# Optimization experiments

Measured on AMD Instinct MI355X. Metric: run time of the kernel, lower is better.

The kernel has to match this reference:

```python
import jax, jax.numpy as jnp
import numpy as np

N_NODES = 20000
L_MAX = 6
R_IN = 256
R_HID = 512
R_OUT = 256
LEAKY_SLOPE = 0.01  # torch.nn.functional.leaky_relu default


def setup_inputs() -> dict:
    key = jax.random.key(0)
    k1, k2, k3, k4 = jax.random.split(key, 4)
    x = jax.random.normal(k1, (N_NODES, R_IN, L_MAX * 2), dtype=jnp.float32)
    # per-node rotation angles -> per-degree 2x2 rotation matrices (k*theta for degree k)
    theta = jax.random.uniform(k2, (N_NODES,), dtype=jnp.float32, minval=0.0, maxval=2.0 * np.pi)
    ang = theta[:, None] * jnp.arange(1, L_MAX + 1, dtype=jnp.float32)[None, :]  # (n, L)
    c, s = jnp.cos(ang), jnp.sin(ang)
    rot_theta = jnp.stack([jnp.stack([c, -s], axis=-1),
                           jnp.stack([s, c], axis=-1)], axis=-2)  # (n, L, 2, 2)
    # xavier_normal: std = sqrt(2 / (fan_in + fan_out))
    W1 = jax.random.normal(k3, (L_MAX, R_HID, R_IN), dtype=jnp.float32) * np.sqrt(2.0 / (R_IN + R_HID))
    W2 = jax.random.normal(k4, (L_MAX, R_OUT, R_HID), dtype=jnp.float32) * np.sqrt(2.0 / (R_HID + R_OUT))
    return {"x": x, "rot_theta": rot_theta, "W1": W1, "W2": W2}


def so2_linear(x, W, r_out):
    # x: (n, r_in, L_max*2); W: (L_max, r_out, r_in)
    n = x.shape[0]
    x4 = x.reshape(n, -1, L_MAX, 2)              # (n, r_in, L, 2)
    out = jnp.einsum('nilc,loi->nolc', x4, W)    # fused block-diagonal GEMM over degrees
    return out.reshape(n, r_out, L_MAX * 2)


def rot_activation(x, rot):
    # rotate each degree-l 2-vector into local frame, apply leaky_relu, rotate back
    n = x.shape[0]
    x4 = x.reshape(n, -1, L_MAX, 2)                      # (n, r, L, 2)
    a = jnp.einsum('njlm,nlmc->njlc', x4, rot)           # x @ R per (node, degree)
    a = jnp.where(a >= 0, a, LEAKY_SLOPE * a)            # pointwise leaky_relu
    out = jnp.einsum('njlc,nlmc->njlm', a, rot)          # (act) @ R^T  (inverse rotation)
    return out.reshape(x.shape)


def reference(x, rot_theta, W1, W2):
    h = so2_linear(x, W1, R_HID)
    h = rot_activation(h, rot_theta)
    return so2_linear(h, W2, R_OUT)
```

## Files before the change

### kernel.cpp

```cpp
#include <hip/hip_runtime.h>
#include <stdint.h>


#define LMAX 6
#define NN 20000
#define RIN 256
#define RHID 512
#define ROUT 256
#define MTILE 64
#define NMT 626
#define MPAD (NMT*MTILE)

typedef __attribute__((ext_vector_type(8))) short short8;
typedef __attribute__((ext_vector_type(16))) float f32x16;

__device__ __forceinline__ uint16_t f2bf(float f) {
  uint32_t x = __builtin_bit_cast(uint32_t, f);
  x += 0x7fffu + ((x >> 16) & 1u);
  return (uint16_t)(x >> 16);
}
__device__ __forceinline__ float bf2f(uint16_t u) {
  return __builtin_bit_cast(float, ((uint32_t)u) << 16);
}

__device__ __forceinline__ f32x16 mfma32(short8 a, short8 b, f32x16 c) {
  return __builtin_amdgcn_mfma_f32_32x32x16_bf16(a, b, c, 0, 0, 0);
}

__device__ __forceinline__ int swz512(int row, int colb) {
  return row * 512 + ((((colb >> 4) ^ row) & 31) << 4) + (colb & 15);
}

__global__ void prep_weights(const float* __restrict__ W1, const float* __restrict__ W2,
                             uint16_t* __restrict__ w1f, uint16_t* __restrict__ w2f) {
  int idx = blockIdx.x * 256 + threadIdx.x;
  if (idx >= LMAX * RHID * RIN) return;
  {
    int l = idx / (RHID * RIN);
    int rem = idx - l * (RHID * RIN);
    int o = rem >> 8;
    int i = rem & 255;
    int lane = ((i >> 3) & 1) * 32 + (o & 31);
    size_t dst = (size_t)l * (RHID * RIN) +
                 ((((size_t)(o >> 5) * 16 + (i >> 4)) * 64 + lane) * 8 + (i & 7));
    w1f[dst] = f2bf(W1[idx]);
  }
  {
    int l = idx / (ROUT * RHID);
    int rem = idx - l * (ROUT * RHID);
    int o = rem >> 9;
    int j = rem & 511;
    int lane = ((j >> 3) & 1) * 32 + (o & 31);
    size_t dst = (size_t)l * (ROUT * RHID) +
                 ((((size_t)(o >> 5) * 32 + (j >> 4)) * 64 + lane) * 8 + (j & 7));
    w2f[dst] = f2bf(W2[idx]);
  }
}

__global__ void prep_x(const float* __restrict__ x, const float* __restrict__ rot,
                       uint16_t* __restrict__ xr) {
  int t = blockIdx.x * 256 + threadIdx.x;
  if (t >= NN * RIN) return;
  int n = t >> 8, i = t & 255;
  const float4* xp = (const float4*)(x + (size_t)t * 12);
  float4 v0 = xp[0], v1 = xp[1], v2 = xp[2];
  float xv[12] = {v0.x, v0.y, v0.z, v0.w, v1.x, v1.y, v1.z, v1.w, v2.x, v2.y, v2.z, v2.w};
  const float* rp = rot + (size_t)n * 24;
#pragma unroll
  for (int l = 0; l < LMAX; ++l) {
    float c0 = xv[2 * l], c1 = xv[2 * l + 1];
    float r00 = rp[4 * l + 0], r01 = rp[4 * l + 1];
    float r10 = rp[4 * l + 2], r11 = rp[4 * l + 3];
    float a0 = c0 * r00 + c1 * r10;
    float a1 = c0 * r01 + c1 * r11;
    size_t base = (size_t)l * MPAD * RIN + (size_t)(2 * n) * RIN + i;
    xr[base] = f2bf(a0);
    xr[base + RIN] = f2bf(a1);
  }
}

__global__ __launch_bounds__(512, 4) void so2_gemm(
    const uint16_t* __restrict__ xr,
    const uint16_t* __restrict__ w1f,
    const uint16_t* __restrict__ w2f,
    uint16_t* __restrict__ g) {
  __shared__ alignas(16) uint8_t Xs[MTILE * 512];
  __shared__ alignas(16) uint8_t A2[MTILE * 512];

  const int l = blockIdx.y;
  const int m0 = blockIdx.x * MTILE;
  const int tid = threadIdx.x;
  const int lane = tid & 63;
  const int wid = tid >> 6;
  const int l31 = lane & 31;
  const int lh = lane >> 5;
  const int wm = wid & 1;
  const int wn4 = wid >> 1;

  const uint16_t* w1p = w1f + (size_t)l * (RHID * RIN);
  const uint16_t* w2p = w2f + (size_t)l * (ROUT * RHID);

  const char* xsrc = (const char*)(xr + (size_t)l * MPAD * RIN + (size_t)m0 * RIN);
#pragma unroll
  for (int it = 0; it < 4; ++it) {
    int off = it * 8192 + tid * 16;
    int row = off >> 9;
    int colb = off & 511;
    short8 v = __builtin_nontemporal_load((const short8*)(xsrc + off));
    *(short8*)(Xs + swz512(row, colb)) = v;
  }
  __syncthreads();

  f32x16 acc1[2];
  f32x16 acc2[2];
#pragma unroll
  for (int a = 0; a < 2; ++a) acc2[a] = (f32x16)(0.f);

  auto G1 = [&](int oc) {
#pragma unroll
    for (int a = 0; a < 2; ++a) acc1[a] = (f32x16)(0.f);
    const uint16_t* wc = w1p + (size_t)(oc * 8 + wid) * (16 * 64 * 8);
#pragma unroll 4
    for (int ks = 0; ks < 16; ++ks) {
      short8 b = *(const short8*)(wc + ((size_t)ks * 64 + lane) * 8);
#pragma unroll
      for (int mf = 0; mf < 2; ++mf) {
        int row = mf * 32 + l31;
        short8 a = *(const short8*)(Xs + swz512(row, ks * 32 + lh * 16));
        acc1[mf] = mfma32(a, b, acc1[mf]);
      }
    }
  };

  auto WA2 = [&]() {
#pragma unroll
    for (int mf = 0; mf < 2; ++mf)
#pragma unroll
      for (int r = 0; r < 16; ++r) {
        int row = mf * 32 + (r & 3) + 8 * (r >> 2) + 4 * lh;
        int colb = (wid * 32 + l31) * 2;
        float v = acc1[mf][r];
        v = v >= 0.f ? v : 0.01f * v;
        *(uint16_t*)(A2 + swz512(row, colb)) = f2bf(v);
      }
  };

  auto G2 = [&](int oc) {
#pragma unroll 4
    for (int ks = 0; ks < 16; ++ks) {
      int row = wm * 32 + l31;
      short8 a = *(const short8*)(A2 + swz512(row, ks * 32 + lh * 16));
#pragma unroll
      for (int nf = 0; nf < 2; ++nf) {
        short8 b = *(const short8*)(w2p +
            ((size_t)((wn4 * 2 + nf) * 32 + oc * 16 + ks) * 64 + lane) * 8);
        acc2[nf] = mfma32(a, b, acc2[nf]);
      }
    }
  };

  G1(0);
  WA2();
  __syncthreads();
  G2(0);
  G1(1);
  __syncthreads();
  WA2();
  __syncthreads();
  G2(1);

#pragma unroll
  for (int nf = 0; nf < 2; ++nf)
#pragma unroll
    for (int r = 0; r < 16; ++r) {
      int row = wm * 32 + (r & 3) + 8 * (r >> 2) + 4 * lh;
      int colb = ((wn4 * 2 + nf) * 32 + l31) * 2;
      *(uint16_t*)(Xs + swz512(row, colb)) = f2bf(acc2[nf][r]);
    }
  __syncthreads();

  char* gdst = (char*)(g + (size_t)l * MPAD * ROUT + (size_t)m0 * ROUT);
#pragma unroll
  for (int it = 0; it < 4; ++it) {
    int off = it * 8192 + tid * 16;
    int row = off >> 9;
    int colb = off & 511;
    short8 v = *(const short8*)(Xs + swz512(row, colb));
    __builtin_nontemporal_store(v, (short8*)(gdst + off));
  }
}

__global__ void post_out(const uint16_t* __restrict__ g, const float* __restrict__ rot,
                         float* __restrict__ out) {
  int n = blockIdx.x;
  int o = threadIdx.x;
  const float* rp = rot + (size_t)n * 24;
  float res[12];
#pragma unroll
  for (int l = 0; l < LMAX; ++l) {
    size_t base = (size_t)l * MPAD * ROUT + (size_t)(2 * n) * ROUT + o;
    float g0 = bf2f(g[base]);
    float g1 = bf2f(g[base + ROUT]);
    res[2 * l]     = rp[4 * l + 0] * g0 + rp[4 * l + 1] * g1;
    res[2 * l + 1] = rp[4 * l + 2] * g0 + rp[4 * l + 3] * g1;
  }
  float4* op = (float4*)(out + (size_t)(n * 256 + o) * 12);
  op[0] = make_float4(res[0], res[1], res[2], res[3]);
  op[1] = make_float4(res[4], res[5], res[6], res[7]);
  op[2] = make_float4(res[8], res[9], res[10], res[11]);
}

extern "C" void kernel_launch(void* const* d_in, const int* in_sizes, int n_in,
                              void* d_out, int out_size, void* d_ws, size_t ws_size,
                              hipStream_t stream) {
  (void)in_sizes; (void)n_in; (void)out_size;
  const float* x   = (const float*)d_in[0];
  const float* rot = (const float*)d_in[1];
  const float* W1  = (const float*)d_in[2];
  const float* W2  = (const float*)d_in[3];
  float* out = (float*)d_out;

  const size_t xr_elems = (size_t)LMAX * MPAD * RIN;
  const size_t w_elems  = (size_t)LMAX * RHID * RIN;
  if (ws_size < (size_t)LMAX * MPAD * ROUT * 2) return;

  uint16_t* xr  = (uint16_t*)d_out;
  uint16_t* w1f = xr + xr_elems;
  uint16_t* w2f = w1f + w_elems;
  uint16_t* g   = (uint16_t*)d_ws;

  prep_weights<<<3072, 256, 0, stream>>>(W1, W2, w1f, w2f);
  prep_x<<<20000, 256, 0, stream>>>(x, rot, xr);
  dim3 gg(NMT, LMAX);
  so2_gemm<<<gg, 512, 0, stream>>>(xr, w1f, w2f, g);
  post_out<<<20000, 256, 0, stream>>>(g, rot, out);
}
```

Measured before the change: 349.8 us.

## Fuse input rotation into GEMM, double M tile, interleave second-layer GEMM with first

Removes the separate prep_x kernel and the bf16 rotated-input intermediate: each GEMM block now reads x and rot directly, rotates the inputs and writes them into LDS. The M tile grows from 64 to 128 rows, so each wave computes a 2x2 fragment block and weight loads are reused across more rows. The grid is reordered so the six degrees of the same node tile run adjacently, which lets them share the x cache lines. The G2(0) and G1(1) loops are merged into one to interleave their MFMAs. The gather from x is strided (two floats per 48-byte row) and launch bounds drop to 2 blocks per CU, which risks poorer load efficiency and lower occupancy.

```diff
diff --git a/kernel.cpp b/kernel.cpp
--- a/kernel.cpp
+++ b/kernel.cpp
@@ -7,9 +7,9 @@
 #define RIN 256
 #define RHID 512
 #define ROUT 256
-#define MTILE 64
-#define NMT 626
-#define MPAD (NMT*MTILE)
+#define MTILE 128
+#define NTILES 313
+#define MPAD (NTILES*MTILE)
 
 typedef __attribute__((ext_vector_type(8))) short short8;
 typedef __attribute__((ext_vector_type(16))) float f32x16;
@@ -57,77 +57,73 @@
   }
 }
 
-__global__ void prep_x(const float* __restrict__ x, const float* __restrict__ rot,
-                       uint16_t* __restrict__ xr) {
-  int t = blockIdx.x * 256 + threadIdx.x;
-  if (t >= NN * RIN) return;
-  int n = t >> 8, i = t & 255;
-  const float4* xp = (const float4*)(x + (size_t)t * 12);
-  float4 v0 = xp[0], v1 = xp[1], v2 = xp[2];
-  float xv[12] = {v0.x, v0.y, v0.z, v0.w, v1.x, v1.y, v1.z, v1.w, v2.x, v2.y, v2.z, v2.w};
-  const float* rp = rot + (size_t)n * 24;
-#pragma unroll
-  for (int l = 0; l < LMAX; ++l) {
-    float c0 = xv[2 * l], c1 = xv[2 * l + 1];
-    float r00 = rp[4 * l + 0], r01 = rp[4 * l + 1];
-    float r10 = rp[4 * l + 2], r11 = rp[4 * l + 3];
-    float a0 = c0 * r00 + c1 * r10;
-    float a1 = c0 * r01 + c1 * r11;
-    size_t base = (size_t)l * MPAD * RIN + (size_t)(2 * n) * RIN + i;
-    xr[base] = f2bf(a0);
-    xr[base + RIN] = f2bf(a1);
-  }
-}
-
-__global__ __launch_bounds__(512, 4) void so2_gemm(
-    const uint16_t* __restrict__ xr,
+__global__ __launch_bounds__(512, 2) void so2_gemm(
+    const float* __restrict__ x,
+    const float* __restrict__ rot,
     const uint16_t* __restrict__ w1f,
     const uint16_t* __restrict__ w2f,
     uint16_t* __restrict__ g) {
   __shared__ alignas(16) uint8_t Xs[MTILE * 512];
   __shared__ alignas(16) uint8_t A2[MTILE * 512];
 
-  const int l = blockIdx.y;
-  const int m0 = blockIdx.x * MTILE;
+  const int l = blockIdx.x;
+  const int tile = blockIdx.y;
+  const int n0 = tile * 64;
   const int tid = threadIdx.x;
   const int lane = tid & 63;
   const int wid = tid >> 6;
   const int l31 = lane & 31;
   const int lh = lane >> 5;
   const int wm = wid & 1;
-  const int wn4 = wid >> 1;
+  const int wn = wid >> 1;
 
   const uint16_t* w1p = w1f + (size_t)l * (RHID * RIN);
   const uint16_t* w2p = w2f + (size_t)l * (ROUT * RHID);
 
-  const char* xsrc = (const char*)(xr + (size_t)l * MPAD * RIN + (size_t)m0 * RIN);
-#pragma unroll
-  for (int it = 0; it < 4; ++it) {
-    int off = it * 8192 + tid * 16;
-    int row = off >> 9;
-    int colb = off & 511;
-    short8 v = __builtin_nontemporal_load((const short8*)(xsrc + off));
-    *(short8*)(Xs + swz512(row, colb)) = v;
-  }
-  __syncthreads();
-
-  f32x16 acc1[2];
-  f32x16 acc2[2];
-#pragma unroll
-  for (int a = 0; a < 2; ++a) acc2[a] = (f32x16)(0.f);
+#pragma unroll 4
+  for (int j = 0; j < 32; ++j) {
+    int p = j * 512 + tid;
+    int nl = p >> 8, i = p & 255;
+    int n = n0 + nl;
+    int ns = n < NN ? n : NN - 1;
+    float c0 = 0.f, c1 = 0.f;
+    if (n < NN) {
+      const float* xp = x + ((size_t)n * 256 + i) * 12 + l * 2;
+      c0 = xp[0]; c1 = xp[1];
+    }
+    const float4 r4 = *(const float4*)(rot + (size_t)ns * 24 + l * 4);
+    float a0 = c0 * r4.x + c1 * r4.z;
+    float a1 = c0 * r4.y + c1 * r4.w;
+    int r0 = nl * 2;
+    *(uint16_t*)(Xs + swz512(r0, i * 2)) = f2bf(a0);
+    *(uint16_t*)(Xs + swz512(r0 + 1, i * 2)) = f2bf(a1);
+  }
+  __syncthreads();
+
+  f32x16 acc1[2][2];
+  f32x16 acc2[2][2];
+#pragma unroll
+  for (int a = 0; a < 2; ++a)
+#pragma unroll
+    for (int b = 0; b < 2; ++b) acc2[a][b] = (f32x16)(0.f);
 
   auto G1 = [&](int oc) {
 #pragma unroll
-    for (int a = 0; a < 2; ++a) acc1[a] = (f32x16)(0.f);
-    const uint16_t* wc = w1p + (size_t)(oc * 8 + wid) * (16 * 64 * 8);
+    for (int a = 0; a < 2; ++a)
+#pragma unroll
+      for (int b = 0; b < 2; ++b) acc1[a][b] = (f32x16)(0.f);
+    const uint16_t* wb0 = w1p + (size_t)(oc * 8 + wn * 2) * (16 * 64 * 8);
+    const uint16_t* wb1 = wb0 + 16 * 64 * 8;
 #pragma unroll 4
     for (int ks = 0; ks < 16; ++ks) {
-      short8 b = *(const short8*)(wc + ((size_t)ks * 64 + lane) * 8);
+      short8 b0 = *(const short8*)(wb0 + ((size_t)ks * 64 + lane) * 8);
+      short8 b1 = *(const short8*)(wb1 + ((size_t)ks * 64 + lane) * 8);
 #pragma unroll
       for (int mf = 0; mf < 2; ++mf) {
-        int row = mf * 32 + l31;
-        short8 a = *(const short8*)(Xs + swz512(row, ks * 32 + lh * 16));
-        acc1[mf] = mfma32(a, b, acc1[mf]);
+        short8 a = *(const short8*)(Xs + swz512((wm * 2 + mf) * 32 + l31,
+                                                ks * 32 + lh * 16));
+        acc1[mf][0] = mfma32(a, b0, acc1[mf][0]);
+        acc1[mf][1] = mfma32(a, b1, acc1[mf][1]);
       }
     }
   };
@@ -136,25 +132,31 @@
 #pragma unroll
     for (int mf = 0; mf < 2; ++mf)
 #pragma unroll
-      for (int r = 0; r < 16; ++r) {
-        int row = mf * 32 + (r & 3) + 8 * (r >> 2) + 4 * lh;
-        int colb = (wid * 32 + l31) * 2;
-        float v = acc1[mf][r];
-        v = v >= 0.f ? v : 0.01f * v;
-        *(uint16_t*)(A2 + swz512(row, colb)) = f2bf(v);
-      }
+      for (int fc = 0; fc < 2; ++fc)
+#pragma unroll
+        for (int r = 0; r < 16; ++r) {
+          int row = (wm * 2 + mf) * 32 + (r & 3) + 8 * (r >> 2) + 4 * lh;
+          int colb = ((wn * 2 + fc) * 32 + l31) * 2;
+          float v = acc1[mf][fc][r];
+          v = v >= 0.f ? v : 0.01f * v;
+          *(uint16_t*)(A2 + swz512(row, colb)) = f2bf(v);
+        }
   };
 
   auto G2 = [&](int oc) {
 #pragma unroll 4
     for (int ks = 0; ks < 16; ++ks) {
-      int row = wm * 32 + l31;
-      short8 a = *(const short8*)(A2 + swz512(row, ks * 32 + lh * 16));
+      short8 a[2];
+#pragma unroll
+      for (int mf = 0; mf < 2; ++mf)
+        a[mf] = *(const short8*)(A2 + swz512((wm * 2 + mf) * 32 + l31,
+                                             ks * 32 + lh * 16));
 #pragma unroll
       for (int nf = 0; nf < 2; ++nf) {
         short8 b = *(const short8*)(w2p +
-            ((size_t)((wn4 * 2 + nf) * 32 + oc * 16 + ks) * 64 + lane) * 8);
-        acc2[nf] = mfma32(a, b, acc2[nf]);
+            ((size_t)((wn * 2 + nf) * 32 + oc * 16 + ks) * 64 + lane) * 8);
+        acc2[0][nf] = mfma32(a[0], b, acc2[0][nf]);
+        acc2[1][nf] = mfma32(a[1], b, acc2[1][nf]);
       }
     }
   };
@@ -162,30 +164,59 @@
   G1(0);
   WA2();
   __syncthreads();
-  G2(0);
-  G1(1);
+
+  {
+#pragma unroll
+    for (int a = 0; a < 2; ++a)
+#pragma unroll
+      for (int b = 0; b < 2; ++b) acc1[a][b] = (f32x16)(0.f);
+    const uint16_t* wb0 = w1p + (size_t)(8 + wn * 2) * (16 * 64 * 8);
+    const uint16_t* wb1 = wb0 + 16 * 64 * 8;
+#pragma unroll 2
+    for (int ks = 0; ks < 16; ++ks) {
+      short8 a20 = *(const short8*)(A2 + swz512((wm * 2) * 32 + l31, ks * 32 + lh * 16));
+      short8 a21 = *(const short8*)(A2 + swz512((wm * 2 + 1) * 32 + l31, ks * 32 + lh * 16));
+#pragma unroll
+      for (int nf = 0; nf < 2; ++nf) {
+        short8 b = *(const short8*)(w2p +
+            ((size_t)((wn * 2 + nf) * 32 + ks) * 64 + lane) * 8);
+        acc2[0][nf] = mfma32(a20, b, acc2[0][nf]);
+        acc2[1][nf] = mfma32(a21, b, acc2[1][nf]);
+      }
+      short8 b0 = *(const short8*)(wb0 + ((size_t)ks * 64 + lane) * 8);
+      short8 b1 = *(const short8*)(wb1 + ((size_t)ks * 64 + lane) * 8);
+#pragma unroll
+      for (int mf = 0; mf < 2; ++mf) {
+        short8 a = *(const short8*)(Xs + swz512((wm * 2 + mf) * 32 + l31,
+                                                ks * 32 + lh * 16));
+        acc1[mf][0] = mfma32(a, b0, acc1[mf][0]);
+        acc1[mf][1] = mfma32(a, b1, acc1[mf][1]);
+      }
+    }
+  }
   __syncthreads();
   WA2();
   __syncthreads();
   G2(1);
-
-#pragma unroll
-  for (int nf = 0; nf < 2; ++nf)
-#pragma unroll
-    for (int r = 0; r < 16; ++r) {
-      int row = wm * 32 + (r & 3) + 8 * (r >> 2) + 4 * lh;
-      int colb = ((wn4 * 2 + nf) * 32 + l31) * 2;
-      *(uint16_t*)(Xs + swz512(row, colb)) = f2bf(acc2[nf][r]);
-    }
-  __syncthreads();
-
-  char* gdst = (char*)(g + (size_t)l * MPAD * ROUT + (size_t)m0 * ROUT);
-#pragma unroll
-  for (int it = 0; it < 4; ++it) {
+  __syncthreads();
+
+#pragma unroll
+  for (int mf = 0; mf < 2; ++mf)
+#pragma unroll
+    for (int nf = 0; nf < 2; ++nf)
+#pragma unroll
+      for (int r = 0; r < 16; ++r) {
+        int row = (wm * 2 + mf) * 32 + (r & 3) + 8 * (r >> 2) + 4 * lh;
+        int col = (wn * 2 + nf) * 32 + l31;
+        *(uint16_t*)(Xs + row * 512 + col * 2) = f2bf(acc2[mf][nf][r]);
+      }
+  __syncthreads();
+
+  char* gdst = (char*)(g + (size_t)l * MPAD * ROUT + (size_t)tile * MTILE * ROUT);
+#pragma unroll
+  for (int it = 0; it < 8; ++it) {
     int off = it * 8192 + tid * 16;
-    int row = off >> 9;
-    int colb = off & 511;
-    short8 v = *(const short8*)(Xs + swz512(row, colb));
+    short8 v = *(const short8*)(Xs + off);
     __builtin_nontemporal_store(v, (short8*)(gdst + off));
   }
 }
@@ -220,18 +251,15 @@
   const float* W2  = (const float*)d_in[3];
   float* out = (float*)d_out;
 
-  const size_t xr_elems = (size_t)LMAX * MPAD * RIN;
-  const size_t w_elems  = (size_t)LMAX * RHID * RIN;
+  const size_t w_elems = (size_t)LMAX * RHID * RIN;
   if (ws_size < (size_t)LMAX * MPAD * ROUT * 2) return;
 
-  uint16_t* xr  = (uint16_t*)d_out;
-  uint16_t* w1f = xr + xr_elems;
+  uint16_t* w1f = (uint16_t*)d_out + 62000000;
   uint16_t* w2f = w1f + w_elems;
   uint16_t* g   = (uint16_t*)d_ws;
 
   prep_weights<<<3072, 256, 0, stream>>>(W1, W2, w1f, w2f);
-  prep_x<<<20000, 256, 0, stream>>>(x, rot, xr);
-  dim3 gg(NMT, LMAX);
-  so2_gemm<<<gg, 512, 0, stream>>>(xr, w1f, w2f, g);
+  dim3 gg(LMAX, NTILES);
+  so2_gemm<<<gg, 512, 0, stream>>>(x, rot, w1f, w2f, g);
   post_out<<<20000, 256, 0, stream>>>(g, rot, out);
 }
```

Measured after the change: 461.1 us. 31.8% more time.
